# Kernel tuning notes

Hardware: AMD Instinct MI355X
Metric: run time of the kernel (lower is better)

The kernel has to match this reference:

```python
import math
import jax, jax.numpy as jnp
import numpy as np

B, S, D = 2, 2048, 1024
H, DK = 16, 64
NUM_BUCKETS = 32
MAX_DISTANCE = 128


def _relative_position_bucket(relative_position, num_buckets=NUM_BUCKETS, max_distance=MAX_DISTANCE):
    # bidirectional=True branch (encoder / non-causal)
    n = -relative_position
    num_buckets = num_buckets // 2
    ret = (n < 0).astype(jnp.int32) * num_buckets
    n = jnp.abs(n)
    max_exact = num_buckets // 2
    is_small = n < max_exact
    # guard log(0); masked out by is_small anyway
    n_safe = jnp.maximum(n, 1).astype(jnp.float32)
    val_if_large = max_exact + (
        jnp.log(n_safe / max_exact) / math.log(max_distance / max_exact) * (num_buckets - max_exact)
    ).astype(jnp.int32)
    val_if_large = jnp.minimum(val_if_large, num_buckets - 1)
    return ret + jnp.where(is_small, n, val_if_large)


def setup_inputs() -> dict:
    key = jax.random.key(0)
    ks = jax.random.split(key, 6)
    std_q = (D * DK) ** -0.5
    std = D ** -0.5
    return {
        "x": jax.random.normal(ks[0], (B, S, D), jnp.float32),
        "q_w": jax.random.normal(ks[1], (H * DK, D), jnp.float32) * std_q,
        "k_w": jax.random.normal(ks[2], (H * DK, D), jnp.float32) * std,
        "v_w": jax.random.normal(ks[3], (H * DK, D), jnp.float32) * std,
        "o_w": jax.random.normal(ks[4], (D, H * DK), jnp.float32) * ((H * DK) ** -0.5),
        "rel_bias": jax.random.normal(ks[5], (NUM_BUCKETS, H), jnp.float32) * std,
    }


def reference(x, q_w, k_w, v_w, o_w, rel_bias):
    b, s, _ = x.shape
    # project and split heads: [B, H, S, DK]
    def proj(w):
        return (x @ w.T).reshape(b, s, H, DK).transpose(0, 2, 1, 3)
    q, k, v = proj(q_w), proj(k_w), proj(v_w)

    # T5-style unscaled attention scores: [B, H, Sq, Sk]
    scores = jnp.einsum("bhqd,bhkd->bhqk", q, k)

    # bucketed relative-position bias
    ctx = jnp.arange(s)[:, None]
    mem = jnp.arange(s)[None, :]
    rp_bucket = _relative_position_bucket(mem - ctx)  # [S, S]
    bias = rel_bias[rp_bucket]                        # [S, S, H]
    bias = bias.transpose(2, 0, 1)[None]              # [1, H, S, S]
    scores = scores + bias

    attn = jax.nn.softmax(scores, axis=-1)
    ctx_out = jnp.einsum("bhqk,bhkd->bhqd", attn, v)
    ctx_out = ctx_out.transpose(0, 2, 1, 3).reshape(b, s, H * DK)
    return ctx_out @ o_w.T
```

## Files before the change

kernel.cpp:

```cpp
#include <hip/hip_runtime.h>
#include <stdint.h>


typedef unsigned short u16;
typedef __attribute__((ext_vector_type(8))) short short8;
typedef __attribute__((ext_vector_type(4))) float float4v;
typedef __attribute__((ext_vector_type(4))) u16 ushort4v;

typedef __attribute__((address_space(1))) void void_g;
typedef __attribute__((address_space(3))) void void_l;

#define L2E 1.4426950408889634f

__device__ __forceinline__ u16 f2b(float f) {
  union { float f; uint32_t u; } v; v.f = f;
  uint32_t r = (v.u + 0x7fffu + ((v.u >> 16) & 1u)) >> 16;
  return (u16)r;
}
__device__ __forceinline__ u16 f2b_fast(float f) {
  union { float f; uint32_t u; } v; v.f = f;
  return (u16)((v.u + 0x8000u) >> 16);
}

__global__ void cvt_all(const float* __restrict__ x,  const float* __restrict__ qw,
                        const float* __restrict__ kw, const float* __restrict__ vw,
                        const float* __restrict__ ow,
                        u16* __restrict__ xb, u16* __restrict__ wqkv, u16* __restrict__ owb) {
  int i = blockIdx.x * blockDim.x + threadIdx.x;
  const float* s; u16* d; int off;
  if (i < 1048576)      { s = x;  d = xb;              off = i; }
  else if (i < 1310720) { s = qw; d = wqkv;            off = i - 1048576; }
  else if (i < 1572864) { s = kw; d = wqkv + 1048576;  off = i - 1310720; }
  else if (i < 1835008) { s = vw; d = wqkv + 2097152;  off = i - 1572864; }
  else                  { s = ow; d = owb;             off = i - 1835008; }
  float4v v = ((const float4v*)s)[off];
  ushort4v o;
  o.x = f2b(v.x); o.y = f2b(v.y); o.z = f2b(v.z); o.w = f2b(v.w);
  ((ushort4v*)d)[off] = o;
}

__global__ void build_bias(const float* __restrict__ rel_bias, float* __restrict__ biasT) {
  int idx = blockIdx.x * blockDim.x + threadIdx.x;
  int h = idx >> 12, t = idx & 4095;
  if (t > 4094) { biasT[h * 4096 + 4095] = -1.0e4f; return; }
  int d = t - 2047;
  int n = -d;
  int ret = (n < 0) ? 16 : 0;
  int na = (n < 0) ? -n : n;
  int bucket;
  if (na < 8) {
    bucket = ret + na;
  } else {
    float v = logf((float)na / 8.0f) / logf(16.0f) * 8.0f;
    int vi = 8 + (int)v;
    bucket = ret + (vi > 15 ? 15 : vi);
  }
  biasT[h * 4096 + t] = (rel_bias[bucket * 16 + h] - 8.0f) * L2E;
}

template<bool OUT_BF16>
__global__ __launch_bounds__(256, 2)
void gemm_bt(const u16* __restrict__ A, const u16* __restrict__ W,
             void* __restrict__ Cp, int K, int N) {
  __shared__ __align__(16) char SM[34816];
  u16* As = (u16*)SM;
  u16* Bs = (u16*)(SM + 8192);
  const int tid = threadIdx.x;
  const int wid = tid >> 6;
  const int lane = tid & 63;
  const int row16 = lane & 15, oct = lane >> 4;
  const int tm = blockIdx.x * 128, tn = blockIdx.y * 128;
  const int wm = (wid & 1) * 64, wn = (wid >> 1) * 64;
  float4v acc[4][4] = {};
  for (int k0 = 0; k0 < K; k0 += 32) {
    __syncthreads();
#pragma unroll
    for (int i = 0; i < 2; i++) {
      const int fo = (i * 256 + tid) * 8;
      const int r = fo >> 5, c = fo & 31;
      __builtin_amdgcn_global_load_lds((void_g*)(A + (size_t)(tm + r) * K + k0 + c),
                                       (void_l*)(As + (i * 256 + wid * 64) * 8), 16, 0, 0);
      __builtin_amdgcn_global_load_lds((void_g*)(W + (size_t)(tn + r) * K + k0 + c),
                                       (void_l*)(Bs + (i * 256 + wid * 64) * 8), 16, 0, 0);
    }
    __syncthreads();
    short8 af[4], bfr[4];
#pragma unroll
    for (int mi = 0; mi < 4; mi++)
      af[mi] = *(const short8*)(As + (wm + mi * 16 + row16) * 32 + oct * 8);
#pragma unroll
    for (int ni = 0; ni < 4; ni++)
      bfr[ni] = *(const short8*)(Bs + (wn + ni * 16 + row16) * 32 + oct * 8);
#pragma unroll
    for (int mi = 0; mi < 4; mi++)
#pragma unroll
      for (int ni = 0; ni < 4; ni++)
        acc[mi][ni] = __builtin_amdgcn_mfma_f32_16x16x32_bf16(af[mi], bfr[ni], acc[mi][ni], 0, 0, 0);
  }

  if (OUT_BF16) {
    u16* Es = (u16*)SM;
    __syncthreads();
#pragma unroll
    for (int mi = 0; mi < 4; mi++)
#pragma unroll
      for (int ni = 0; ni < 4; ni++)
#pragma unroll
        for (int r = 0; r < 4; r++)
          Es[(wm + mi * 16 + oct * 4 + r) * 136 + wn + ni * 16 + row16] = f2b(acc[mi][ni][r]);
    __syncthreads();
    u16* C = (u16*)Cp;
#pragma unroll
    for (int it = 0; it < 8; it++) {
      int idx = it * 256 + tid;
      int row = idx >> 4, c = idx & 15;
      short8 v = *(const short8*)(Es + row * 136 + c * 8);
      *(short8*)(C + (size_t)(tm + row) * N + tn + c * 8) = v;
    }
  } else {
    float* Ef = (float*)SM;
    float* C = (float*)Cp;
#pragma unroll
    for (int pass = 0; pass < 2; pass++) {
      __syncthreads();
      if ((wid & 1) == pass) {
#pragma unroll
        for (int mi = 0; mi < 4; mi++)
#pragma unroll
          for (int ni = 0; ni < 4; ni++)
#pragma unroll
            for (int r = 0; r < 4; r++)
              Ef[(mi * 16 + oct * 4 + r) * 132 + wn + ni * 16 + row16] = acc[mi][ni][r];
      }
      __syncthreads();
#pragma unroll
      for (int it = 0; it < 8; it++) {
        int idx = it * 256 + tid;
        int row = idx >> 5, c = idx & 31;
        float4v v = *(const float4v*)(Ef + row * 132 + c * 4);
        *(float4v*)(C + (size_t)(tm + pass * 64 + row) * N + tn + c * 4) = v;
      }
    }
  }
}

__global__ __launch_bounds__(256, 2)
void transpose_v(const u16* __restrict__ QKV, u16* __restrict__ vTp) {
  const int s0 = blockIdx.x * 64, h = blockIdx.y, b = blockIdx.z;
  const int tid = threadIdx.x;
  __shared__ u16 T[64 * 73];
  const u16* src = QKV + 2048 + (size_t)b * 2048 * 3072 + h * 64;
#pragma unroll
  for (int it = 0; it < 2; it++) {
    int idx = it * 256 + tid;
    int sl = idx >> 3;
    int c = idx & 7;
    short8 v = *(const short8*)(src + (size_t)(s0 + sl) * 3072 + c * 8);
#pragma unroll
    for (int k = 0; k < 8; k++) T[(c * 8 + k) * 73 + sl] = (u16)v[k];
  }
  __syncthreads();
  u16* dst = vTp + ((size_t)(b * 16 + h) * 64) * 2048 + s0;
#pragma unroll
  for (int it = 0; it < 2; it++) {
    int idx = it * 256 + tid;
    int d = idx >> 3;
    int cs = idx & 7;
    short8 o;
#pragma unroll
    for (int k = 0; k < 8; k++) {
      int sp = cs * 8 + k;
      int sl = (sp & 32) + 16 * (sp & 1) + ((sp & 31) >> 1);
      o[k] = (short)T[d * 73 + sl];
    }
    *(short8*)(dst + (size_t)d * 2048 + cs * 8) = o;
  }
}

__global__ __launch_bounds__(256, 2)
void flash_attn(const u16* __restrict__ QKV, const u16* __restrict__ vTp,
                const float* __restrict__ biasT, u16* __restrict__ ctx) {
  const int S = 2048, LDQ = 3072;
  const int qt0 = blockIdx.x * 128;
  const int h = blockIdx.y, b = blockIdx.z;
  const int tid = threadIdx.x, wid = tid >> 6, lane = tid & 63;
  const int row16 = lane & 15, oct = lane >> 4;

  __shared__ __align__(16) float biasS[2176];
  __shared__ __align__(16) u16 Ks[2][64][40];
  __shared__ __align__(16) u16 Vts[2][64][40];
  __shared__ __align__(16) u16 Pl[4][2][16][40];

  {
    const float* bsrc = biasT + h * 4096 + (1920 - qt0);
    for (int i = tid; i < 544; i += 256)
      ((float4v*)biasS)[i] = ((const float4v*)bsrc)[i];
  }

  const u16* qbase = QKV + ((size_t)b * S + qt0 + wid * 32) * LDQ + h * 64;
  short8 qf[2][2];
#pragma unroll
  for (int f = 0; f < 2; f++)
#pragma unroll
    for (int hd = 0; hd < 2; hd++)
      qf[f][hd] = *(const short8*)(qbase + (size_t)(f * 16 + row16) * LDQ + hd * 32 + oct * 8);

  float l_r[2][4] = {};
  float4v o_acc[2][4] = {};

  const int sr = lane >> 2, c8 = (lane & 3) * 8;
  const int srow = wid * 16 + sr;
  const u16* Kst = QKV + 1024 + ((size_t)b * S + srow) * LDQ + h * 64 + c8;
  const u16* Vst = vTp + ((size_t)(b * 16 + h) * 64 + srow) * 2048 + c8;

  short8 kreg[2], vreg[2];
#pragma unroll
  for (int hd = 0; hd < 2; hd++) kreg[hd] = *(const short8*)(Kst + hd * 32);
#pragma unroll
  for (int ks = 0; ks < 2; ks++) vreg[ks] = *(const short8*)(Vst + ks * 32);

  for (int kt = 0; kt < S; kt += 64) {
    __syncthreads();
#pragma unroll
    for (int hd = 0; hd < 2; hd++) *(short8*)&Ks[hd][srow][c8] = kreg[hd];
#pragma unroll
    for (int ks = 0; ks < 2; ks++) *(short8*)&Vts[ks][srow][c8] = vreg[ks];
    __syncthreads();

    if (kt + 64 < S) {
#pragma unroll
      for (int hd = 0; hd < 2; hd++)
        kreg[hd] = *(const short8*)(Kst + (size_t)(kt + 64) * LDQ + hd * 32);
#pragma unroll
      for (int ks = 0; ks < 2; ks++)
        vreg[ks] = *(const short8*)(Vst + (kt + 64) + ks * 32);
    }

    short8 kf[4][2];
#pragma unroll
    for (int st = 0; st < 4; st++)
#pragma unroll
      for (int hd = 0; hd < 2; hd++)
        kf[st][hd] = *(const short8*)&Ks[hd][st * 16 + row16][oct * 8];

    float4v sc[2][4];
#pragma unroll
    for (int f = 0; f < 2; f++)
#pragma unroll
      for (int st = 0; st < 4; st++) {
        float4v s = {};
        s = __builtin_amdgcn_mfma_f32_16x16x32_bf16(qf[f][0], kf[st][0], s, 0, 0, 0);
        s = __builtin_amdgcn_mfma_f32_16x16x32_bf16(qf[f][1], kf[st][1], s, 0, 0, 0);
        sc[f][st] = s;
      }

    short8 vf[2][4];
#pragma unroll
    for (int ks = 0; ks < 2; ks++)
#pragma unroll
      for (int ni = 0; ni < 4; ni++)
        vf[ks][ni] = *(const short8*)&Vts[ks][ni * 16 + row16][oct * 8];

#pragma unroll
    for (int f = 0; f < 2; f++) {
      const int base = kt + row16 - wid * 32 - f * 16 - oct * 4 + 127;
#pragma unroll
      for (int r = 0; r < 4; r++) {
        const int i0 = base - r;
        float b0 = biasS[i0],      b1 = biasS[i0 + 16];
        float b2 = biasS[i0 + 32], b3 = biasS[i0 + 48];
        sc[f][0][r] = __builtin_amdgcn_exp2f(__builtin_fmaf(sc[f][0][r], L2E, b0));
        sc[f][1][r] = __builtin_amdgcn_exp2f(__builtin_fmaf(sc[f][1][r], L2E, b1));
        sc[f][2][r] = __builtin_amdgcn_exp2f(__builtin_fmaf(sc[f][2][r], L2E, b2));
        sc[f][3][r] = __builtin_amdgcn_exp2f(__builtin_fmaf(sc[f][3][r], L2E, b3));
      }
      if (f == 0) {
#pragma unroll
        for (int ks = 0; ks < 2; ks++)
#pragma unroll
          for (int r = 0; r < 4; r++) {
            uint32_t pk = (uint32_t)f2b_fast(sc[0][2 * ks][r]) |
                          ((uint32_t)f2b_fast(sc[0][2 * ks + 1][r]) << 16);
            *(uint32_t*)&Pl[wid][ks][oct * 4 + r][2 * row16] = pk;
          }
      }
    }
#pragma unroll
    for (int f = 0; f < 2; f++) {
      if (f == 1) {
#pragma unroll
        for (int ks = 0; ks < 2; ks++)
#pragma unroll
          for (int r = 0; r < 4; r++) {
            uint32_t pk = (uint32_t)f2b_fast(sc[1][2 * ks][r]) |
                          ((uint32_t)f2b_fast(sc[1][2 * ks + 1][r]) << 16);
            *(uint32_t*)&Pl[wid][ks][oct * 4 + r][2 * row16] = pk;
          }
      }
#pragma unroll
      for (int r = 0; r < 4; r++)
        l_r[f][r] += (sc[f][0][r] + sc[f][1][r]) + (sc[f][2][r] + sc[f][3][r]);
#pragma unroll
      for (int ks = 0; ks < 2; ks++) {
        short8 pf = *(const short8*)&Pl[wid][ks][row16][oct * 8];
#pragma unroll
        for (int ni = 0; ni < 4; ni++)
          o_acc[f][ni] = __builtin_amdgcn_mfma_f32_16x16x32_bf16(pf, vf[ks][ni], o_acc[f][ni], 0, 0, 0);
      }
    }
  }

#pragma unroll
  for (int f = 0; f < 2; f++) {
#pragma unroll
    for (int r = 0; r < 4; r++) {
      float v = l_r[f][r];
      v += __shfl_xor(v, 1); v += __shfl_xor(v, 2);
      v += __shfl_xor(v, 4); v += __shfl_xor(v, 8);
      l_r[f][r] = 1.0f / v;
    }
    const size_t orow = (size_t)b * S + qt0 + wid * 32 + f * 16 + oct * 4;
#pragma unroll
    for (int ni = 0; ni < 4; ni++)
#pragma unroll
      for (int r = 0; r < 4; r++)
        ctx[(orow + r) * 1024 + h * 64 + ni * 16 + row16] = f2b_fast(o_acc[f][ni][r] * l_r[f][r]);
  }
}

extern "C" void kernel_launch(void* const* d_in, const int* in_sizes, int n_in,
                              void* d_out, int out_size, void* d_ws, size_t ws_size,
                              hipStream_t stream) {
  const float* x        = (const float*)d_in[0];
  const float* q_w      = (const float*)d_in[1];
  const float* k_w      = (const float*)d_in[2];
  const float* v_w      = (const float*)d_in[3];
  const float* o_w      = (const float*)d_in[4];
  const float* rel_bias = (const float*)d_in[5];

  char* ws = (char*)d_ws;
  u16*   xb    = (u16*)(ws);
  u16*   wqkv  = (u16*)(ws + 8388608);
  u16*   owb   = (u16*)(ws + 14680064);
  u16*   qkvb  = (u16*)(ws + 16777216);
  u16*   ctxb  = (u16*)(ws + 41943040);
  float* biasT = (float*)(ws + 50331648);
  u16*   vTp   = xb;

  cvt_all<<<8192, 256, 0, stream>>>(x, q_w, k_w, v_w, o_w, xb, wqkv, owb);
  build_bias<<<256, 256, 0, stream>>>(rel_bias, biasT);

  dim3 g1(4096 / 128, 3072 / 128);
  gemm_bt<true><<<g1, 256, 0, stream>>>(xb, wqkv, qkvb, 1024, 3072);

  dim3 gt(2048 / 64, 16, 2);
  transpose_v<<<gt, 256, 0, stream>>>(qkvb, vTp);

  dim3 g2(2048 / 128, 16, 2);
  flash_attn<<<g2, 256, 0, stream>>>(qkvb, vTp, biasT, ctxb);

  dim3 g3(4096 / 128, 1024 / 128);
  gemm_bt<false><<<g3, 256, 0, stream>>>(ctxb, owb, d_out, 1024, 1024);
}
```

Measured before the change: 204.8 us.

## Double GEMM K-step to 64 and fold bias build into conversion kernel

The GEMM main loop now stages a 64-wide K slice per iteration instead of 32. It uses a k-split LDS layout of two 32-column sub-tiles and runs two MFMA sub-steps per barrier pair, which halves the number of syncthreads and global-load rounds. Separately, the relative-bias table construction is merged into the bf16 conversion kernel as extra blocks, removing one kernel launch. LDS use grows to 32 KB per block and stays inside the existing 34816-byte allocation.

Result: faster. 195.8 us (-4.4%).

```diff
diff --git a/kernel.cpp b/kernel.cpp
--- a/kernel.cpp
+++ b/kernel.cpp
@@ -24,9 +24,30 @@
 
 __global__ void cvt_all(const float* __restrict__ x,  const float* __restrict__ qw,
                         const float* __restrict__ kw, const float* __restrict__ vw,
-                        const float* __restrict__ ow,
-                        u16* __restrict__ xb, u16* __restrict__ wqkv, u16* __restrict__ owb) {
-  int i = blockIdx.x * blockDim.x + threadIdx.x;
+                        const float* __restrict__ ow, const float* __restrict__ rel_bias,
+                        u16* __restrict__ xb, u16* __restrict__ wqkv, u16* __restrict__ owb,
+                        float* __restrict__ biasT) {
+  int bi = blockIdx.x;
+  if (bi >= 8192) {
+    int idx = (bi - 8192) * 256 + threadIdx.x;
+    int h = idx >> 12, t = idx & 4095;
+    if (t > 4094) { biasT[h * 4096 + 4095] = -1.0e4f; return; }
+    int d = t - 2047;
+    int n = -d;
+    int ret = (n < 0) ? 16 : 0;
+    int na = (n < 0) ? -n : n;
+    int bucket;
+    if (na < 8) {
+      bucket = ret + na;
+    } else {
+      float v = logf((float)na / 8.0f) / logf(16.0f) * 8.0f;
+      int vi = 8 + (int)v;
+      bucket = ret + (vi > 15 ? 15 : vi);
+    }
+    biasT[h * 4096 + t] = (rel_bias[bucket * 16 + h] - 8.0f) * L2E;
+    return;
+  }
+  int i = bi * 256 + threadIdx.x;
   const float* s; u16* d; int off;
   if (i < 1048576)      { s = x;  d = xb;              off = i; }
   else if (i < 1310720) { s = qw; d = wqkv;            off = i - 1048576; }
@@ -39,63 +60,52 @@
   ((ushort4v*)d)[off] = o;
 }
 
-__global__ void build_bias(const float* __restrict__ rel_bias, float* __restrict__ biasT) {
-  int idx = blockIdx.x * blockDim.x + threadIdx.x;
-  int h = idx >> 12, t = idx & 4095;
-  if (t > 4094) { biasT[h * 4096 + 4095] = -1.0e4f; return; }
-  int d = t - 2047;
-  int n = -d;
-  int ret = (n < 0) ? 16 : 0;
-  int na = (n < 0) ? -n : n;
-  int bucket;
-  if (na < 8) {
-    bucket = ret + na;
-  } else {
-    float v = logf((float)na / 8.0f) / logf(16.0f) * 8.0f;
-    int vi = 8 + (int)v;
-    bucket = ret + (vi > 15 ? 15 : vi);
-  }
-  biasT[h * 4096 + t] = (rel_bias[bucket * 16 + h] - 8.0f) * L2E;
-}
-
 template<bool OUT_BF16>
 __global__ __launch_bounds__(256, 2)
 void gemm_bt(const u16* __restrict__ A, const u16* __restrict__ W,
              void* __restrict__ Cp, int K, int N) {
   __shared__ __align__(16) char SM[34816];
   u16* As = (u16*)SM;
-  u16* Bs = (u16*)(SM + 8192);
+  u16* Bs = (u16*)(SM + 16384);
   const int tid = threadIdx.x;
   const int wid = tid >> 6;
   const int lane = tid & 63;
   const int row16 = lane & 15, oct = lane >> 4;
   const int tm = blockIdx.x * 128, tn = blockIdx.y * 128;
   const int wm = (wid & 1) * 64, wn = (wid >> 1) * 64;
+  const int srow = lane >> 2;
+  const int sc = (lane & 3) * 8;
   float4v acc[4][4] = {};
-  for (int k0 = 0; k0 < K; k0 += 32) {
-    __syncthreads();
-#pragma unroll
-    for (int i = 0; i < 2; i++) {
-      const int fo = (i * 256 + tid) * 8;
-      const int r = fo >> 5, c = fo & 31;
+  for (int k0 = 0; k0 < K; k0 += 64) {
+    __syncthreads();
+#pragma unroll
+    for (int i = 0; i < 4; i++) {
+      const int idx = i * 4 + wid;
+      const int kk = idx & 1;
+      const int rb = idx >> 1;
+      const int r = rb * 16 + srow;
+      const int c = kk * 32 + sc;
       __builtin_amdgcn_global_load_lds((void_g*)(A + (size_t)(tm + r) * K + k0 + c),
-                                       (void_l*)(As + (i * 256 + wid * 64) * 8), 16, 0, 0);
+                                       (void_l*)(As + (kk * 128 + rb * 16) * 32), 16, 0, 0);
       __builtin_amdgcn_global_load_lds((void_g*)(W + (size_t)(tn + r) * K + k0 + c),
-                                       (void_l*)(Bs + (i * 256 + wid * 64) * 8), 16, 0, 0);
-    }
-    __syncthreads();
-    short8 af[4], bfr[4];
-#pragma unroll
-    for (int mi = 0; mi < 4; mi++)
-      af[mi] = *(const short8*)(As + (wm + mi * 16 + row16) * 32 + oct * 8);
-#pragma unroll
-    for (int ni = 0; ni < 4; ni++)
-      bfr[ni] = *(const short8*)(Bs + (wn + ni * 16 + row16) * 32 + oct * 8);
-#pragma unroll
-    for (int mi = 0; mi < 4; mi++)
+                                       (void_l*)(Bs + (kk * 128 + rb * 16) * 32), 16, 0, 0);
+    }
+    __syncthreads();
+#pragma unroll
+    for (int kk = 0; kk < 2; kk++) {
+      short8 af[4], bfr[4];
+#pragma unroll
+      for (int mi = 0; mi < 4; mi++)
+        af[mi] = *(const short8*)(As + (kk * 128 + wm + mi * 16 + row16) * 32 + oct * 8);
 #pragma unroll
       for (int ni = 0; ni < 4; ni++)
-        acc[mi][ni] = __builtin_amdgcn_mfma_f32_16x16x32_bf16(af[mi], bfr[ni], acc[mi][ni], 0, 0, 0);
+        bfr[ni] = *(const short8*)(Bs + (kk * 128 + wn + ni * 16 + row16) * 32 + oct * 8);
+#pragma unroll
+      for (int mi = 0; mi < 4; mi++)
+#pragma unroll
+        for (int ni = 0; ni < 4; ni++)
+          acc[mi][ni] = __builtin_amdgcn_mfma_f32_16x16x32_bf16(af[mi], bfr[ni], acc[mi][ni], 0, 0, 0);
+    }
   }
 
   if (OUT_BF16) {
@@ -347,8 +357,8 @@
   float* biasT = (float*)(ws + 50331648);
   u16*   vTp   = xb;
 
-  cvt_all<<<8192, 256, 0, stream>>>(x, q_w, k_w, v_w, o_w, xb, wqkv, owb);
-  build_bias<<<256, 256, 0, stream>>>(rel_bias, biasT);
+  cvt_all<<<8448, 256, 0, stream>>>(x, q_w, k_w, v_w, o_w, rel_bias,
+                                    xb, wqkv, owb, biasT);
 
   dim3 g1(4096 / 128, 3072 / 128);
   gemm_bt<true><<<g1, 256, 0, stream>>>(xb, wqkv, qkvb, 1024, 3072);
```
